# Kernel optimization log

Measured on AMD Instinct MI355X. Metric: run time of the kernel, lower is better.

The kernel has to match this reference:

```python
import jax, jax.numpy as jnp
from jax import lax
import numpy as np

T = 3          # boundary_kernel_size -> band width / dilation iterations
SDF_K = 3.0
ALPHA = 0.25   # focal alpha
GAMMA = 2.0    # focal gamma
TEMP = 1.5     # adaptive weighting temperature
SMOOTH = 1e-6  # iou smooth
EPS = 1e-12


def _maxpool3(x):
    # 3x3 max pool, stride 1, SAME padding on [B, H, W]
    return lax.reduce_window(x, -jnp.inf, lax.max, (1, 3, 3), (1, 1, 1), 'SAME')


def _bce_logits(x, t):
    # stable binary_cross_entropy_with_logits, elementwise
    return jnp.maximum(x, 0.0) - x * t + jnp.log1p(jnp.exp(-jnp.abs(x)))


def _limited_distance(mask, max_d):
    # iterative 3x3 dilation -> truncated distance-to-mask, values in {0..max_d, max_d+1}
    covered = mask > 0.5
    dist = jnp.where(covered, 0.0, float(max_d + 1)).astype(jnp.float32)
    for d in range(1, max_d + 1):
        covered_new = _maxpool3(covered.astype(jnp.float32)) > 0
        newly = jnp.logical_and(jnp.logical_not(covered), covered_new)
        dist = jnp.where(newly, float(d), dist)
        covered = covered_new
    return dist


def _boundary_loss(logits, target):
    p = jax.nn.sigmoid(logits)
    tb = (target > 0.5).astype(logits.dtype)
    outside_dist = _limited_distance(tb, T)        # distance to foreground
    inside_dist = _limited_distance(1.0 - tb, T)   # distance to background
    sdf = jnp.where(tb > 0.5, inside_dist, -outside_dist)
    band = (jnp.abs(sdf) <= float(T)).astype(logits.dtype)
    weight = (1.0 - jnp.abs(jnp.tanh(sdf / SDF_K))) * band
    pc = jnp.clip(p, EPS, 1.0 - EPS)
    bce = -(tb * jnp.log(pc) + (1.0 - tb) * jnp.log(1.0 - pc))
    denom = jnp.maximum(jnp.sum(weight, axis=(1, 2)), 1.0)
    return jnp.mean(jnp.sum(bce * weight, axis=(1, 2)) / denom)


def _focal_loss(logits, target):
    x = logits.reshape(logits.shape[0], -1)
    t = target.reshape(target.shape[0], -1)
    p = jax.nn.sigmoid(x)
    ce = _bce_logits(x, t)
    p_t = p * t + (1.0 - p) * (1.0 - t)
    loss = ce * (1.0 - p_t) ** GAMMA
    alpha_t = ALPHA * t + (1.0 - ALPHA) * (1.0 - t)
    loss = alpha_t * loss
    return jnp.mean(jnp.mean(loss, axis=1))


def _iou_loss(logits, target):
    p = jax.nn.sigmoid(logits).reshape(logits.shape[0], -1)
    t = target.reshape(target.shape[0], -1)
    inter = jnp.sum(p * t, axis=-1)
    union = jnp.sum(p, axis=-1) + jnp.sum(t, axis=-1) - inter
    iou = (inter + SMOOTH) / (union + SMOOTH)
    return jnp.mean(1.0 - iou)


def _dice_loss(logits, target):
    p = jax.nn.sigmoid(logits).reshape(logits.shape[0], -1)
    t = target.reshape(target.shape[0], -1)
    inter = jnp.sum(p * t, axis=-1)
    dice = (2.0 * inter + 1.0) / (jnp.sum(p, axis=-1) + jnp.sum(t, axis=-1) + 1.0)
    return jnp.mean(1.0 - dice)


def setup_inputs() -> dict:
    key = jax.random.key(0)
    k1, k2 = jax.random.split(key)
    B, H, W = 32, 1024, 1024
    pred = jax.random.normal(k1, (B, H, W), dtype=jnp.float32) * 2.0
    targets = (jax.random.uniform(k2, (B, H, W)) > 0.7).astype(jnp.float32)
    log_vars = jnp.log(jnp.array([1.0, 1.0, 0.5, 0.3, 0.2], dtype=jnp.float32))
    return {'pred': pred, 'targets': targets, 'log_vars': log_vars}


def reference(pred, targets, log_vars):
    target = targets.astype(pred.dtype)
    # 5 component losses, each pre-scaled by loss_scaling_factors
    ce = jnp.mean(_bce_logits(pred, target))                      # * 1.0
    dice = _dice_loss(pred, target)                               # * 1.0
    focal = 0.5 * _focal_loss(pred, target)
    iou = 0.3 * _iou_loss(pred, target)
    bnd = 0.2 * _boundary_loss(pred, target)
    losses = jnp.stack([ce, dice, focal, iou, bnd])
    # adaptive weighting (eval mode): normalized sigmoid of log_vars / temperature
    raw = jax.nn.sigmoid(log_vars / TEMP)
    weights = raw / jnp.sum(raw) * raw.shape[0]
    total = jnp.sum(weights * losses)
    return total
```

## Files before the change

### kernel.cpp

```cpp
#include <hip/hip_runtime.h>
#include <stdint.h>

#define HW    1024
#define BATCH 32
#define TR    16
#define HR    (TR + 6)
#define WN    32
#define TILES (HW / TR)
#define NBLK  (BATCH * TILES)

#define W1 0.6784872f
#define W2 0.4172171f
#define W3 0.2384058f

__global__ __launch_bounds__(256) void k_main(const float* __restrict__ pred,
                                              const float* __restrict__ targ,
                                              float* __restrict__ ws) {
    __shared__ uint32_t fg[HR][WN];
    __shared__ uint4 plane[TR][WN];
    __shared__ float red[4][8];

    const int bid  = blockIdx.x;
    const int blk  = (bid & 7) * (NBLK / 8) + (bid >> 3);
    const int b    = blk / TILES;
    const int tile = blk - b * TILES;
    const int r0   = tile * TR;
    const int tid  = threadIdx.x;
    const int lane = tid & 63;
    const int wid  = tid >> 6;

    const float4* p4 = (const float4*)(pred + (size_t)b * HW * HW + (size_t)r0 * HW);
    float4 xa = p4[tid];
    float4 xb = p4[256 + tid];

    for (int i = tid; i < HR * WN; i += 256) (&fg[0][0])[i] = 0u;
    __syncthreads();

    const float* tbase = targ + (size_t)b * HW * HW;
    for (int task = wid; task < HR * 4; task += 4) {
        const int row = task >> 2;
        const int g   = task & 3;
        const int gr  = r0 - 3 + row;
        if (gr >= 0 && gr < HW) {
            const float4 t4 = *(const float4*)(tbase + (size_t)gr * HW + (g << 8) + (lane << 2));
            const uint32_t u0 = __float_as_uint(t4.x), u1 = __float_as_uint(t4.y);
            const uint32_t u2 = __float_as_uint(t4.z), u3 = __float_as_uint(t4.w);
            const uint32_t n = ((u0 >> 23) & 1u) | ((u1 >> 22) & 2u)
                             | ((u2 >> 21) & 4u) | ((u3 >> 20) & 8u);
            uint32_t v = n << ((lane & 7) << 2);
            v |= __shfl_xor(v, 1);
            v |= __shfl_xor(v, 2);
            v |= __shfl_xor(v, 4);
            if ((lane & 7) == 0) fg[row][(g << 3) + (lane >> 3)] = v;
        }
    }
    __syncthreads();

    for (int i = tid; i < TR * WN; i += 256) {
        const int row = i >> 5;
        const int wz  = i & 31;
        const int hr  = row + 3;
        uint32_t v1c = 0, v2c = 0, v3c = 0, v1p = 0, v2p = 0, v3p = 0, v1n = 0, v2n = 0, v3n = 0;
        uint32_t u1c = 0, u2c = 0, u3c = 0, u1p = 0, u2p = 0, u3p = 0, u1n = 0, u2n = 0, u3n = 0;
        uint32_t tw = 0;
#pragma unroll
        for (int dr = -3; dr <= 3; ++dr) {
            const int r  = hr + dr;
            const int gr = r0 - 3 + r;
            const bool valid = (gr >= 0) && (gr < HW);
            const uint32_t c = fg[r][wz];
            const uint32_t p = (wz > 0)  ? fg[r][wz - 1] : 0u;
            const uint32_t n = (wz < 31) ? fg[r][wz + 1] : 0u;
            const uint32_t cb = valid ? ~c : 0u;
            const uint32_t pb = (valid && wz > 0)  ? ~p : 0u;
            const uint32_t nb = (valid && wz < 31) ? ~n : 0u;
            if (dr == 0) tw = c;
            v3c |= c;  v3p |= p;  v3n |= n;
            u3c |= cb; u3p |= pb; u3n |= nb;
            if (dr >= -2 && dr <= 2) {
                v2c |= c;  v2p |= p;  v2n |= n;
                u2c |= cb; u2p |= pb; u2n |= nb;
            }
            if (dr >= -1 && dr <= 1) {
                v1c |= c;  v1p |= p;  v1n |= n;
                u1c |= cb; u1p |= pb; u1n |= nb;
            }
        }
        const uint32_t d1f = v1c | (v1c << 1) | (v1p >> 31) | (v1c >> 1) | (v1n << 31);
        const uint32_t d2f = v2c | (v2c << 1) | (v2p >> 31) | (v2c >> 1) | (v2n << 31)
                                 | (v2c << 2) | (v2p >> 30) | (v2c >> 2) | (v2n << 30);
        const uint32_t d3f = v3c | (v3c << 1) | (v3p >> 31) | (v3c >> 1) | (v3n << 31)
                                 | (v3c << 2) | (v3p >> 30) | (v3c >> 2) | (v3n << 30)
                                 | (v3c << 3) | (v3p >> 29) | (v3c >> 3) | (v3n << 29);
        const uint32_t d1b = u1c | (u1c << 1) | (u1p >> 31) | (u1c >> 1) | (u1n << 31);
        const uint32_t d2b = u2c | (u2c << 1) | (u2p >> 31) | (u2c >> 1) | (u2n << 31)
                                 | (u2c << 2) | (u2p >> 30) | (u2c >> 2) | (u2n << 30);
        const uint32_t d3b = u3c | (u3c << 1) | (u3p >> 31) | (u3c >> 1) | (u3n << 31)
                                 | (u3c << 2) | (u3p >> 30) | (u3c >> 2) | (u3n << 30)
                                 | (u3c << 3) | (u3p >> 29) | (u3c >> 3) | (u3n << 29);
        uint4 pl;
        pl.x = tw;
        pl.y = (tw & d1b) | (~tw & d1f);
        pl.z = (tw & d2b) | (~tw & d2f);
        pl.w = (tw & d3b) | (~tw & d3f);
        plane[row][wz] = pl;
    }
    __syncthreads();

    float s_pt = 0.f, s_p = 0.f, s_t = 0.f, s_w = 0.f, s_bw = 0.f, s_ce = 0.f, s_f = 0.f;
    const int wz = tid >> 3;
    const int sh = (tid & 7) << 2;

    for (int rr = 0; rr < TR; ++rr) {
        const float4 cur = xa;
        xa = xb;
        if (rr + 2 < TR) xb = p4[(rr + 2) * 256 + tid];
        const uint4 pl = plane[rr][wz];
        const uint32_t tn = (pl.x >> sh) & 0xFu;
        const uint32_t n1 = (pl.y >> sh) & 0xFu;
        const uint32_t n2 = (pl.z >> sh) & 0xFu;
        const uint32_t n3 = (pl.w >> sh) & 0xFu;
#pragma unroll
        for (int j = 0; j < 4; ++j) {
            const float x = ((const float*)&cur)[j];
            const uint32_t tb = (tn >> j) & 1u;
            const float tf = (float)tb;

            const float ax  = fabsf(x);
            const float e   = __expf(-ax);
            const float opl = 1.f + e;
            const float inv = __builtin_amdgcn_rcpf(opl);
            const float l1p = __logf(opl);
            const float ce  = fmaxf(x, 0.f) - x * tf + l1p;
            const float pm  = 1.f - inv;
            const float p   = (x >= 0.f) ? inv : pm;
            const float omp = tb ? (1.f - p) : p;
            const float at  = tb ? 0.25f : 0.75f;
            const float fo  = ce * omp * omp * at;

            const float f1 = (float)((n1 >> j) & 1u);
            const float f2 = (float)((n2 >> j) & 1u);
            const float f3 = (float)((n3 >> j) & 1u);
            const float w  = fmaf(f1, W1 - W2, fmaf(f2, W2 - W3, f3 * W3));

            s_ce += ce;
            s_f  += fo;
            s_p  += p;
            s_pt  = fmaf(tf, p, s_pt);
            s_t  += tf;
            s_w  += w;
            s_bw  = fmaf(w, ce, s_bw);
        }
    }

    float v[7] = {s_pt, s_p, s_t, s_w, s_bw, s_ce, s_f};
#pragma unroll
    for (int off = 1; off < 64; off <<= 1) {
#pragma unroll
        for (int j = 0; j < 7; ++j) v[j] += __shfl_xor(v[j], off);
    }
    if (lane == 0) {
#pragma unroll
        for (int j = 0; j < 7; ++j) red[wid][j] = v[j];
    }
    __syncthreads();
    if (tid < 7) {
        float s = red[0][tid] + red[1][tid] + red[2][tid] + red[3][tid];
        ws[tid * NBLK + blk] = s;
    }
}

__global__ __launch_bounds__(TILES) void k_reduce(const float* __restrict__ ws,
                                                  float* __restrict__ res) {
    __shared__ float sm[TILES];
    const int b = blockIdx.x;
    const int t = threadIdx.x;
    for (int q = 0; q < 7; ++q) {
        sm[t] = ws[q * NBLK + b * TILES + t];
        __syncthreads();
        for (int s = TILES / 2; s > 0; s >>= 1) {
            if (t < s) sm[t] += sm[t + s];
            __syncthreads();
        }
        if (t == 0) res[q * BATCH + b] = sm[0];
        __syncthreads();
    }
}

__global__ __launch_bounds__(64) void k_final(const float* __restrict__ res,
                                              const float* __restrict__ lv,
                                              float* __restrict__ out) {
    const int lane = threadIdx.x;
    float d = 0.f, io = 0.f, bn = 0.f;
    if (lane < 32) {
        const float pt = res[0 * 32 + lane];
        const float p  = res[1 * 32 + lane];
        const float t  = res[2 * 32 + lane];
        const float w  = res[3 * 32 + lane];
        const float bw = res[4 * 32 + lane];
        d  = 1.f - (2.f * pt + 1.f) / (p + t + 1.f);
        io = 1.f - (pt + 1e-6f) / (p + t - pt + 1e-6f);
        bn = bw / fmaxf(w, 1.f);
    }
#pragma unroll
    for (int off = 1; off < 32; off <<= 1) {
        d  += __shfl_xor(d, off);
        io += __shfl_xor(io, off);
        bn += __shfl_xor(bn, off);
    }
    if (lane == 0) {
        float ce_sum = 0.f, f_sum = 0.f;
        for (int bb = 0; bb < 32; ++bb) {
            ce_sum += res[5 * 32 + bb];
            f_sum  += res[6 * 32 + bb];
        }
        const float N = 33554432.f;
        float ls[5];
        ls[0] = ce_sum / N;
        ls[1] = d * (1.f / 32.f);
        ls[2] = 0.5f * f_sum / N;
        ls[3] = 0.3f * io * (1.f / 32.f);
        ls[4] = 0.2f * bn * (1.f / 32.f);
        float r[5], s = 0.f;
#pragma unroll
        for (int i = 0; i < 5; ++i) {
            r[i] = 1.f / (1.f + __expf(-lv[i] * (1.f / 1.5f)));
            s += r[i];
        }
        float tot = 0.f;
#pragma unroll
        for (int i = 0; i < 5; ++i) tot += (r[i] / s) * 5.f * ls[i];
        out[0] = tot;
    }
}

extern "C" void kernel_launch(void* const* d_in, const int* in_sizes, int n_in,
                              void* d_out, int out_size, void* d_ws, size_t ws_size,
                              hipStream_t stream) {
    const float* pred = (const float*)d_in[0];
    const float* targ = (const float*)d_in[1];
    const float* lv   = (const float*)d_in[2];
    float* out = (float*)d_out;
    float* ws  = (float*)d_ws;
    float* res = ws + 7 * NBLK;

    k_main<<<NBLK, 256, 0, stream>>>(pred, targ, ws);
    k_reduce<<<BATCH, TILES, 0, stream>>>(ws, res);
    k_final<<<1, 64, 0, stream>>>(res, lv, out);
}
```

Baseline: 81.41 us.

## Pack elementwise math into float2 FMAs, popcount counts, merge tail kernels

```diff
diff --git a/kernel.cpp b/kernel.cpp
--- a/kernel.cpp
+++ b/kernel.cpp
@@ -12,6 +12,12 @@
 #define W1 0.6784872f
 #define W2 0.4172171f
 #define W3 0.2384058f
+
+typedef float v2f __attribute__((ext_vector_type(2)));
+
+static __device__ __forceinline__ v2f pk_fma(v2f a, v2f b, v2f c) {
+    return __builtin_elementwise_fma(a, b, c);
+}
 
 __global__ __launch_bounds__(256) void k_main(const float* __restrict__ pred,
                                               const float* __restrict__ targ,
@@ -33,29 +39,28 @@
     float4 xa = p4[tid];
     float4 xb = p4[256 + tid];
 
-    for (int i = tid; i < HR * WN; i += 256) (&fg[0][0])[i] = 0u;
-    __syncthreads();
-
     const float* tbase = targ + (size_t)b * HW * HW;
     for (int task = wid; task < HR * 4; task += 4) {
         const int row = task >> 2;
         const int g   = task & 3;
         const int gr  = r0 - 3 + row;
+        uint32_t v = 0u;
         if (gr >= 0 && gr < HW) {
             const float4 t4 = *(const float4*)(tbase + (size_t)gr * HW + (g << 8) + (lane << 2));
             const uint32_t u0 = __float_as_uint(t4.x), u1 = __float_as_uint(t4.y);
             const uint32_t u2 = __float_as_uint(t4.z), u3 = __float_as_uint(t4.w);
             const uint32_t n = ((u0 >> 23) & 1u) | ((u1 >> 22) & 2u)
                              | ((u2 >> 21) & 4u) | ((u3 >> 20) & 8u);
-            uint32_t v = n << ((lane & 7) << 2);
-            v |= __shfl_xor(v, 1);
-            v |= __shfl_xor(v, 2);
-            v |= __shfl_xor(v, 4);
-            if ((lane & 7) == 0) fg[row][(g << 3) + (lane >> 3)] = v;
-        }
-    }
-    __syncthreads();
-
+            v = n << ((lane & 7) << 2);
+        }
+        v |= __shfl_xor(v, 1);
+        v |= __shfl_xor(v, 2);
+        v |= __shfl_xor(v, 4);
+        if ((lane & 7) == 0) fg[row][(g << 3) + (lane >> 3)] = v;
+    }
+    __syncthreads();
+
+    uint32_t ct = 0, c1 = 0, c2 = 0, c3 = 0;
     for (int i = tid; i < TR * WN; i += 256) {
         const int row = i >> 5;
         const int wz  = i & 31;
@@ -104,56 +109,84 @@
         pl.z = (tw & d2b) | (~tw & d2f);
         pl.w = (tw & d3b) | (~tw & d3f);
         plane[row][wz] = pl;
-    }
-    __syncthreads();
-
-    float s_pt = 0.f, s_p = 0.f, s_t = 0.f, s_w = 0.f, s_bw = 0.f, s_ce = 0.f, s_f = 0.f;
+        ct += __popc(pl.x);
+        c1 += __popc(pl.y);
+        c2 += __popc(pl.z);
+        c3 += __popc(pl.w);
+    }
+    __syncthreads();
+
+    v2f a_pt = {0.f, 0.f}, a_p = {0.f, 0.f}, a_bw = {0.f, 0.f},
+        a_ce = {0.f, 0.f}, a_f = {0.f, 0.f};
     const int wz = tid >> 3;
     const int sh = (tid & 7) << 2;
+
+    const v2f dW12 = {W1 - W2, W1 - W2};
+    const v2f dW23 = {W2 - W3, W2 - W3};
+    const v2f cW3  = {W3, W3};
+    const v2f kM2  = {-2.f, -2.f};
+    const v2f kP1  = {1.f, 1.f};
+    const v2f kMH  = {-0.5f, -0.5f};
+    const v2f k34  = {0.75f, 0.75f};
 
     for (int rr = 0; rr < TR; ++rr) {
         const float4 cur = xa;
         xa = xb;
         if (rr + 2 < TR) xb = p4[(rr + 2) * 256 + tid];
         const uint4 pl = plane[rr][wz];
-        const uint32_t tn = (pl.x >> sh) & 0xFu;
-        const uint32_t n1 = (pl.y >> sh) & 0xFu;
-        const uint32_t n2 = (pl.z >> sh) & 0xFu;
-        const uint32_t n3 = (pl.w >> sh) & 0xFu;
-#pragma unroll
-        for (int j = 0; j < 4; ++j) {
-            const float x = ((const float*)&cur)[j];
-            const uint32_t tb = (tn >> j) & 1u;
-            const float tf = (float)tb;
-
-            const float ax  = fabsf(x);
-            const float e   = __expf(-ax);
-            const float opl = 1.f + e;
-            const float inv = __builtin_amdgcn_rcpf(opl);
-            const float l1p = __logf(opl);
-            const float ce  = fmaxf(x, 0.f) - x * tf + l1p;
-            const float pm  = 1.f - inv;
-            const float p   = (x >= 0.f) ? inv : pm;
-            const float omp = tb ? (1.f - p) : p;
-            const float at  = tb ? 0.25f : 0.75f;
-            const float fo  = ce * omp * omp * at;
-
-            const float f1 = (float)((n1 >> j) & 1u);
-            const float f2 = (float)((n2 >> j) & 1u);
-            const float f3 = (float)((n3 >> j) & 1u);
-            const float w  = fmaf(f1, W1 - W2, fmaf(f2, W2 - W3, f3 * W3));
-
-            s_ce += ce;
-            s_f  += fo;
-            s_p  += p;
-            s_pt  = fmaf(tf, p, s_pt);
-            s_t  += tf;
-            s_w  += w;
-            s_bw  = fmaf(w, ce, s_bw);
-        }
-    }
-
-    float v[7] = {s_pt, s_p, s_t, s_w, s_bw, s_ce, s_f};
+#pragma unroll
+        for (int h = 0; h < 2; ++h) {
+            v2f x;
+            x.x = (h == 0) ? cur.x : cur.z;
+            x.y = (h == 0) ? cur.y : cur.w;
+            const int q0 = sh + (h << 1);
+
+            v2f tf = {(float)((pl.x >> q0) & 1u), (float)((pl.x >> (q0 + 1)) & 1u)};
+            v2f f1 = {(float)((pl.y >> q0) & 1u), (float)((pl.y >> (q0 + 1)) & 1u)};
+            v2f f2 = {(float)((pl.z >> q0) & 1u), (float)((pl.z >> (q0 + 1)) & 1u)};
+            v2f f3 = {(float)((pl.w >> q0) & 1u), (float)((pl.w >> (q0 + 1)) & 1u)};
+
+            v2f ea;
+            ea.x = fabsf(x.x) * -1.4426950408889634f;
+            ea.y = fabsf(x.y) * -1.4426950408889634f;
+            v2f e   = {__builtin_amdgcn_exp2f(ea.x), __builtin_amdgcn_exp2f(ea.y)};
+            v2f opl = e + 1.0f;
+            v2f inv = {__builtin_amdgcn_rcpf(opl.x), __builtin_amdgcn_rcpf(opl.y)};
+            v2f lg  = {__builtin_amdgcn_logf(opl.x), __builtin_amdgcn_logf(opl.y)};
+            v2f l1p = lg * 0.6931471805599453f;
+            v2f pm  = 1.0f - inv;
+            v2f p;
+            p.x = (x.x >= 0.f) ? inv.x : pm.x;
+            p.y = (x.y >= 0.f) ? inv.y : pm.y;
+
+            v2f mx;
+            mx.x = fmaxf(x.x, 0.f);
+            mx.y = fmaxf(x.y, 0.f);
+            v2f ce  = pk_fma(x, -tf, mx + l1p);
+
+            v2f m2p = pk_fma(p, kM2, kP1);
+            v2f omp = pk_fma(tf, m2p, p);
+            v2f at  = pk_fma(tf, kMH, k34);
+            v2f o2  = omp * omp;
+            a_f  = pk_fma(o2 * at, ce, a_f);
+
+            v2f w = pk_fma(f1, dW12, pk_fma(f2, dW23, f3 * cW3));
+            a_bw = pk_fma(w, ce, a_bw);
+            a_ce += ce;
+            a_p  += p;
+            a_pt  = pk_fma(tf, p, a_pt);
+        }
+    }
+
+    float v[7];
+    v[0] = a_pt.x + a_pt.y;
+    v[1] = a_p.x + a_p.y;
+    v[2] = (float)ct;
+    v[3] = fmaf((float)c1, W1 - W2,
+           fmaf((float)c2, W2 - W3, (float)c3 * W3));
+    v[4] = a_bw.x + a_bw.y;
+    v[5] = a_ce.x + a_ce.y;
+    v[6] = a_f.x + a_f.y;
 #pragma unroll
     for (int off = 1; off < 64; off <<= 1) {
 #pragma unroll
@@ -170,67 +203,62 @@
     }
 }
 
-__global__ __launch_bounds__(TILES) void k_reduce(const float* __restrict__ ws,
-                                                  float* __restrict__ res) {
-    __shared__ float sm[TILES];
-    const int b = blockIdx.x;
-    const int t = threadIdx.x;
-    for (int q = 0; q < 7; ++q) {
-        sm[t] = ws[q * NBLK + b * TILES + t];
-        __syncthreads();
-        for (int s = TILES / 2; s > 0; s >>= 1) {
-            if (t < s) sm[t] += sm[t + s];
-            __syncthreads();
-        }
-        if (t == 0) res[q * BATCH + b] = sm[0];
-        __syncthreads();
-    }
-}
-
-__global__ __launch_bounds__(64) void k_final(const float* __restrict__ res,
+__global__ __launch_bounds__(256) void k_tail(const float* __restrict__ ws,
                                               const float* __restrict__ lv,
                                               float* __restrict__ out) {
-    const int lane = threadIdx.x;
-    float d = 0.f, io = 0.f, bn = 0.f;
-    if (lane < 32) {
-        const float pt = res[0 * 32 + lane];
-        const float p  = res[1 * 32 + lane];
-        const float t  = res[2 * 32 + lane];
-        const float w  = res[3 * 32 + lane];
-        const float bw = res[4 * 32 + lane];
-        d  = 1.f - (2.f * pt + 1.f) / (p + t + 1.f);
-        io = 1.f - (pt + 1e-6f) / (p + t - pt + 1e-6f);
-        bn = bw / fmaxf(w, 1.f);
-    }
-#pragma unroll
-    for (int off = 1; off < 32; off <<= 1) {
-        d  += __shfl_xor(d, off);
-        io += __shfl_xor(io, off);
-        bn += __shfl_xor(bn, off);
-    }
-    if (lane == 0) {
-        float ce_sum = 0.f, f_sum = 0.f;
-        for (int bb = 0; bb < 32; ++bb) {
-            ce_sum += res[5 * 32 + bb];
-            f_sum  += res[6 * 32 + bb];
-        }
-        const float N = 33554432.f;
-        float ls[5];
-        ls[0] = ce_sum / N;
-        ls[1] = d * (1.f / 32.f);
-        ls[2] = 0.5f * f_sum / N;
-        ls[3] = 0.3f * io * (1.f / 32.f);
-        ls[4] = 0.2f * bn * (1.f / 32.f);
-        float r[5], s = 0.f;
-#pragma unroll
-        for (int i = 0; i < 5; ++i) {
-            r[i] = 1.f / (1.f + __expf(-lv[i] * (1.f / 1.5f)));
-            s += r[i];
-        }
-        float tot = 0.f;
-#pragma unroll
-        for (int i = 0; i < 5; ++i) tot += (r[i] / s) * 5.f * ls[i];
-        out[0] = tot;
+    __shared__ float res[7][BATCH];
+    const int tid = threadIdx.x;
+    const int b   = tid >> 3;
+    const int g   = tid & 7;
+#pragma unroll
+    for (int q = 0; q < 7; ++q) {
+        float s = 0.f;
+#pragma unroll
+        for (int i = 0; i < TILES / 8; ++i) s += ws[q * NBLK + b * TILES + g + i * 8];
+        s += __shfl_xor(s, 1);
+        s += __shfl_xor(s, 2);
+        s += __shfl_xor(s, 4);
+        if (g == 0) res[q][b] = s;
+    }
+    __syncthreads();
+    if (tid < 32) {
+        const float pt = res[0][tid];
+        const float p  = res[1][tid];
+        const float t  = res[2][tid];
+        const float w  = res[3][tid];
+        const float bw = res[4][tid];
+        float d  = 1.f - (2.f * pt + 1.f) / (p + t + 1.f);
+        float io = 1.f - (pt + 1e-6f) / (p + t - pt + 1e-6f);
+        float bn = bw / fmaxf(w, 1.f);
+        float ce = res[5][tid];
+        float fo = res[6][tid];
+#pragma unroll
+        for (int off = 1; off < 32; off <<= 1) {
+            d  += __shfl_xor(d, off);
+            io += __shfl_xor(io, off);
+            bn += __shfl_xor(bn, off);
+            ce += __shfl_xor(ce, off);
+            fo += __shfl_xor(fo, off);
+        }
+        if (tid == 0) {
+            const float N = 33554432.f;
+            float ls[5];
+            ls[0] = ce / N;
+            ls[1] = d * (1.f / 32.f);
+            ls[2] = 0.5f * fo / N;
+            ls[3] = 0.3f * io * (1.f / 32.f);
+            ls[4] = 0.2f * bn * (1.f / 32.f);
+            float r[5], s = 0.f;
+#pragma unroll
+            for (int i = 0; i < 5; ++i) {
+                r[i] = 1.f / (1.f + __expf(-lv[i] * (1.f / 1.5f)));
+                s += r[i];
+            }
+            float tot = 0.f;
+#pragma unroll
+            for (int i = 0; i < 5; ++i) tot += (r[i] / s) * 5.f * ls[i];
+            out[0] = tot;
+        }
     }
 }
 
@@ -242,9 +270,7 @@
     const float* lv   = (const float*)d_in[2];
     float* out = (float*)d_out;
     float* ws  = (float*)d_ws;
-    float* res = ws + 7 * NBLK;
 
     k_main<<<NBLK, 256, 0, stream>>>(pred, targ, ws);
-    k_reduce<<<BATCH, TILES, 0, stream>>>(ws, res);
-    k_final<<<1, 64, 0, stream>>>(res, lv, out);
-}
+    k_tail<<<1, 256, 0, stream>>>(ws, lv, out);
+}
```

Measured after the change: 76.13 us. 6.5% less time.
